# Performance work log

Hardware: AMD Instinct MI355X
Metric: run time of the kernel (lower is better)

The kernel has to match this reference:

```python
import jax, jax.numpy as jnp
import numpy as np

NEG_INF = -1e30  # stand-in for -inf in additive causal mask (softmax-safe)


def rotary_pos_emb(x):
    # x: [B, T, H, D]. Faithful to source: freqs = 1/1000**(arange(0,D,2)//D)
    # with INTEGER floor division -> exponent 0 -> all freqs == 1.0.
    B, T, H, D = x.shape
    exponents = (jnp.arange(0, D, 2)[: D // 2] // D).astype(jnp.float32)
    freqs = 1.0 / jnp.power(jnp.float32(1000.0), exponents)          # [D/2]
    theta = jnp.arange(T, dtype=jnp.float32)[:, None] * freqs[None, :]  # [T, D/2]
    cos = jnp.cos(theta)[None, :, None, :]  # [1, T, 1, D/2]
    sin = jnp.sin(theta)[None, :, None, :]
    xr = x.astype(jnp.float32).reshape(B, T, H, D // 2, 2)
    x0, x1 = xr[..., 0], xr[..., 1]
    # complex multiply (x0 + i x1) * (cos + i sin)
    out = jnp.stack([x0 * cos - x1 * sin, x0 * sin + x1 * cos], axis=-1)
    return out.reshape(B, T, H, D).astype(x.dtype)


def attention_fwd(x, wq, wk, wv, wo, n_heads=32):
    B, T, C = x.shape
    hd = C // n_heads  # head_dim = 128
    # nn.Linear(bias=False): y = x @ W^T with W: [out, in]
    xq = (x @ wq.T).reshape(B, T, n_heads, hd)
    xk = (x @ wk.T).reshape(B, T, n_heads, hd)
    xv = (x @ wv.T).reshape(B, T, n_heads, hd)
    xq = rotary_pos_emb(xq)
    xk = rotary_pos_emb(xk)
    # n_rep == 1 -> repeat_kv is identity
    scale = hd ** -0.5
    scores = jnp.einsum('bqhd,bkhd->bhqk', xq, xk) * scale  # [B,H,T,T]
    causal = jnp.tril(jnp.ones((T, T), dtype=bool))
    scores = jnp.where(causal[None, None], scores, NEG_INF)
    probs = jax.nn.softmax(scores.astype(jnp.float32), axis=-1).astype(xq.dtype)
    out = jnp.einsum('bhqk,bkhd->bqhd', probs, xv).reshape(B, T, C)
    return out @ wo.T


def setup_inputs() -> dict:
    key = jax.random.key(0)
    ks = jax.random.split(key, 5)
    B, T, C = 2, 2048, 4096
    s = 0.02
    return {
        'x': jax.random.normal(ks[0], (B, T, C), jnp.float32),
        'wq': jax.random.normal(ks[1], (C, C), jnp.float32) * s,
        'wk': jax.random.normal(ks[2], (C, C), jnp.float32) * s,
        'wv': jax.random.normal(ks[3], (C, C), jnp.float32) * s,
        'wo': jax.random.normal(ks[4], (C, C), jnp.float32) * s,
    }


def reference(x, wq, wk, wv, wo):
    return attention_fwd(x, wq, wk, wv, wo)
```

## Files before the change

kernel.cpp:

```cpp
#include <hip/hip_runtime.h>
#include <hip/hip_bf16.h>
#include <stdint.h>

typedef __bf16 bf16_t;
typedef __attribute__((ext_vector_type(8))) __bf16 bf16x8;
typedef __attribute__((ext_vector_type(4))) float f32x4;

#define GLL16(gptr, lptr)                                                      \
  __builtin_amdgcn_global_load_lds(                                            \
      (__attribute__((address_space(1))) void*)(gptr),                         \
      (__attribute__((address_space(3))) void*)(lptr), 16, 0, 0)

__global__ __launch_bounds__(256) void cast5_kernel(const float* __restrict__ x,
                                                    const float* __restrict__ wq,
                                                    const float* __restrict__ wk,
                                                    const float* __restrict__ wv,
                                                    const float* __restrict__ wo,
                                                    bf16_t* __restrict__ outbase) {
  const size_t SZ = (size_t)4096 * 4096;
  const float* in;
  switch (blockIdx.y) {
    case 0: in = x; break;
    case 1: in = wq; break;
    case 2: in = wk; break;
    case 3: in = wv; break;
    default: in = wo; break;
  }
  bf16_t* out = outbase + (size_t)blockIdx.y * SZ;
  int i = blockIdx.x * 256 + threadIdx.x;
  const float4* p = (const float4*)in + (size_t)i * 2;
  float4 a = p[0], b = p[1];
  bf16x8 o;
  o[0] = (__bf16)a.x; o[1] = (__bf16)a.y; o[2] = (__bf16)a.z; o[3] = (__bf16)a.w;
  o[4] = (__bf16)b.x; o[5] = (__bf16)b.y; o[6] = (__bf16)b.z; o[7] = (__bf16)b.w;
  *((bf16x8*)out + i) = o;
}

#define STAGE_HALF(gbase, ldsbase)                                             \
  do {                                                                         \
    GLL16((gbase) + (size_t)(w * 32 + sr) * 4096 + sq, (ldsbase) + w * 1024);  \
    GLL16((gbase) + (size_t)(w * 32 + 16 + sr) * 4096 + sq,                    \
          (ldsbase) + w * 1024 + 512);                                         \
  } while (0)

#define MFMA_CL(ACCB_, AF_, BF_)                                               \
  __builtin_amdgcn_sched_barrier(0);                                           \
  __builtin_amdgcn_s_setprio(1);                                               \
  _Pragma("unroll") for (int mi = 0; mi < 4; ++mi)                             \
      _Pragma("unroll") for (int ni = 0; ni < 4; ++ni)                         \
          acc[(ACCB_) + mi][ni] = __builtin_amdgcn_mfma_f32_16x16x32_bf16(     \
              AF_[mi], BF_[ni], acc[(ACCB_) + mi][ni], 0, 0, 0);               \
  __builtin_amdgcn_s_setprio(0);

#define KITER(P_, AF0C_, BFC_, AF0N_, BFN_, KT_, MORE_)                        \
  do {                                                                         \
    _Pragma("unroll") for (int mi = 0; mi < 4; ++mi) af1t[mi] =                \
        *(const bf16x8*)&As[P_][(wr * 128 + 64 + mi * 16 + l15) * 32 + sl8];   \
    MFMA_CL(0, AF0C_, BFC_)                                                    \
    asm volatile("s_waitcnt lgkmcnt(0)" ::: "memory");                         \
    __builtin_amdgcn_sched_barrier(0);                                         \
    __builtin_amdgcn_s_barrier();    \
    if (MORE_) {                                                               \
      STAGE_HALF(Ag + (size_t)(KT_ + 2) * 32, &As[P_][0]);                     \
      STAGE_HALF(Bg + (size_t)(KT_ + 2) * 32, &Bs[P_][0]);                     \
      asm volatile("s_waitcnt vmcnt(4)" ::: "memory");                         \
    } else {                                                                   \
      asm volatile("s_waitcnt vmcnt(0)" ::: "memory");                         \
    }                                                                          \
    __builtin_amdgcn_s_barrier();                \
    _Pragma("unroll") for (int ni = 0; ni < 4; ++ni) BFN_[ni] =                \
        *(const bf16x8*)&Bs[P_ ^ 1][(wc * 64 + ni * 16 + l15) * 32 + sl8];     \
    _Pragma("unroll") for (int mi = 0; mi < 4; ++mi) AF0N_[mi] =               \
        *(const bf16x8*)&As[P_ ^ 1][(wr * 128 + mi * 16 + l15) * 32 + sl8];    \
    MFMA_CL(4, af1t, BFC_)                                                     \
  } while (0)

#define GEMM256_MAIN(Aptr, Bptr)                                               \
  const bf16_t* Ag = (Aptr) + (size_t)bm * 4096;                               \
  const bf16_t* Bg = (Bptr) + (size_t)bn * 4096;                               \
  f32x4 acc[8][4] = {};                                                        \
  bf16x8 af0A[4], af0B[4], bfA[4], bfB[4], af1t[4];                            \
  STAGE_HALF(Ag, &As[0][0]);                                                   \
  STAGE_HALF(Bg, &Bs[0][0]);                                                   \
  STAGE_HALF(Ag + 32, &As[1][0]);                                              \
  STAGE_HALF(Bg + 32, &Bs[1][0]);                                              \
  asm volatile("s_waitcnt vmcnt(4)" ::: "memory");           \
  __builtin_amdgcn_s_barrier();                                                \
  _Pragma("unroll") for (int ni = 0; ni < 4; ++ni) bfA[ni] =                   \
      *(const bf16x8*)&Bs[0][(wc * 64 + ni * 16 + l15) * 32 + sl8];            \
  _Pragma("unroll") for (int mi = 0; mi < 4; ++mi) af0A[mi] =                  \
      *(const bf16x8*)&As[0][(wr * 128 + mi * 16 + l15) * 32 + sl8];           \
  for (int jj = 0; jj < 64; ++jj) {                                            \
    const int kt = jj * 2;                                                     \
    const bool m = (jj < 63);                                                  \
    KITER(0, af0A, bfA, af0B, bfB, kt, m);                                     \
    KITER(1, af0B, bfB, af0A, bfA, kt + 1, m);                                 \
  }

__device__ __forceinline__ void epi_rope256(const f32x4 (&acc)[8][4],
                                            bf16_t* __restrict__ C, int bm,
                                            int bn, int wr, int wc, int quad,
                                            int l15) {
#pragma unroll
  for (int a = 0; a < 8; ++a) {
    const int row0 = bm + wr * 128 + (a & 3) * 16 + (a >> 2) * 64 + quad * 4;
    float fsv[4], fcv[4];
#pragma unroll
    for (int r = 0; r < 4; ++r)
      sincosf((float)((row0 + r) & 2047), &fsv[r], &fcv[r]);
#pragma unroll
    for (int ni = 0; ni < 4; ++ni) {
      const int col = bn + wc * 64 + ni * 16 + l15;
      const bool odd = (col & 1);
#pragma unroll
      for (int r = 0; r < 4; ++r) {
        float v = acc[a][ni][r];
        float pr = __shfl_xor(v, 1, 64);
        float o = odd ? (pr * fsv[r] + v * fcv[r]) : (v * fcv[r] - pr * fsv[r]);
        C[(size_t)(row0 + r) * 4096 + col] = (__bf16)o;
      }
    }
  }
}

__device__ __forceinline__ void epi_vt256(const f32x4 (&acc)[8][4],
                                          bf16_t* __restrict__ VT, int bm,
                                          int bn, int wr, int wc, int quad,
                                          int l15) {
#pragma unroll
  for (int a = 0; a < 8; ++a) {
    const int row0 = bm + wr * 128 + (a & 3) * 16 + (a >> 2) * 64 + quad * 4;
    const int b = row0 >> 11, t0 = row0 & 2047;
#pragma unroll
    for (int ni = 0; ni < 4; ++ni) {
      const int col = bn + wc * 64 + ni * 16 + l15;
      const int h = col >> 7, d = col & 127;
      union { __bf16 e[4]; uint2 u; } pk;
#pragma unroll
      for (int r = 0; r < 4; ++r) pk.e[r] = (__bf16)acc[a][ni][r];
      *(uint2*)&VT[((size_t)((b * 32 + h) * 128 + d)) * 2048 + t0] = pk.u;
    }
  }
}

__global__ __launch_bounds__(512, 2) void gemm_qkv(const bf16_t* __restrict__ X,
                                                   const bf16_t* __restrict__ WQ,
                                                   const bf16_t* __restrict__ WK,
                                                   const bf16_t* __restrict__ WV,
                                                   bf16_t* __restrict__ Qo,
                                                   bf16_t* __restrict__ Ko,
                                                   bf16_t* __restrict__ VTo) {
  __shared__ bf16_t As[2][8192];
  __shared__ bf16_t Bs[2][8192];
  const int tid = threadIdx.x;
  const int w = tid >> 6;
  const int lane = tid & 63;
  const int quad = lane >> 4;
  const int l15 = lane & 15;
  const int wr = w >> 2, wc = w & 3;
  const int sr = lane >> 2;
  const int sq = (((lane & 3) ^ ((lane >> 3) & 3))) * 8;
  const int sl8 = (quad ^ ((l15 >> 1) & 3)) * 8;
  const int mat = blockIdx.y;
  int id = blockIdx.x;
  id = (id & 7) * 32 + (id >> 3);
  const int bm = (id >> 4) * 256, bn = (id & 15) * 256;
  const bf16_t* Bp = (mat == 0) ? WQ : (mat == 1) ? WK : WV;

  GEMM256_MAIN(X, Bp)

  if (mat == 0)
    epi_rope256(acc, Qo, bm, bn, wr, wc, quad, l15);
  else if (mat == 1)
    epi_rope256(acc, Ko, bm, bn, wr, wc, quad, l15);
  else
    epi_vt256(acc, VTo, bm, bn, wr, wc, quad, l15);
}

__global__ __launch_bounds__(512, 2) void gemm_out(const bf16_t* __restrict__ A,
                                                   const bf16_t* __restrict__ B,
                                                   float* __restrict__ C) {
  __shared__ bf16_t As[2][8192];
  __shared__ bf16_t Bs[2][8192];
  const int tid = threadIdx.x;
  const int w = tid >> 6;
  const int lane = tid & 63;
  const int quad = lane >> 4;
  const int l15 = lane & 15;
  const int wr = w >> 2, wc = w & 3;
  const int sr = lane >> 2;
  const int sq = (((lane & 3) ^ ((lane >> 3) & 3))) * 8;
  const int sl8 = (quad ^ ((l15 >> 1) & 3)) * 8;
  int id = blockIdx.x;
  id = (id & 7) * 32 + (id >> 3);
  const int bm = (id >> 4) * 256, bn = (id & 15) * 256;

  GEMM256_MAIN(A, B)

#pragma unroll
  for (int a = 0; a < 8; ++a) {
    const int row0 = bm + wr * 128 + (a & 3) * 16 + (a >> 2) * 64 + quad * 4;
#pragma unroll
    for (int ni = 0; ni < 4; ++ni) {
      const int col = bn + wc * 64 + ni * 16 + l15;
#pragma unroll
      for (int r = 0; r < 4; ++r)
        C[(size_t)(row0 + r) * 4096 + col] = acc[a][ni][r];
    }
  }
}

__global__ __launch_bounds__(256) void attn_kernel(const bf16_t* __restrict__ Q,
                                                   const bf16_t* __restrict__ Km,
                                                   const bf16_t* __restrict__ VT,
                                                   bf16_t* __restrict__ O) {
  __shared__ bf16_t Ks[64 * 128];
  __shared__ bf16_t Vts[128 * 64];
  __shared__ bf16_t QPs[64 * 128];
  const int tid = threadIdx.x;
  const int w = tid >> 6;
  const int lane = tid & 63;
  const int quad = lane >> 4;
  const int l15 = lane & 15;
  const int bh = blockIdx.x;
  const int qtile = 31 - blockIdx.y;
  const int mrow_base = (bh >> 5) * 2048;
  const int h = bh & 31;
  const float scale = 0.08838834764831845f;

#pragma unroll
  for (int it = 0; it < 4; ++it) {
    int c = w * 4 + it;
    int row = c * 4 + (lane >> 4);
    int cc = (lane & 15) ^ (row & 15);
    GLL16(Q + (size_t)(mrow_base + qtile * 64 + row) * 4096 + h * 128 + cc * 8,
          &QPs[c * 512]);
  }
  __syncthreads();
  bf16x8 qf[4];
#pragma unroll
  for (int ks = 0; ks < 4; ++ks) {
    int row = w * 16 + l15;
    int slot = (ks * 4 + quad) ^ (row & 15);
    qf[ks] = *(const bf16x8*)&QPs[row * 128 + slot * 8];
  }
  bf16_t* Pw = &QPs[w * 16 * 72];

  f32x4 accO[8] = {};
  float mrun[4], lrun[4];
#pragma unroll
  for (int r = 0; r < 4; ++r) { mrun[r] = -1e30f; lrun[r] = 0.f; }

  for (int kt = 0; kt <= qtile; ++kt) {
    __syncthreads();
#pragma unroll
    for (int it = 0; it < 4; ++it) {
      int c = w * 4 + it;
      int krow = c * 4 + (lane >> 4);
      int kcc = (lane & 15) ^ (krow & 15);
      GLL16(Km + (size_t)(mrow_base + kt * 64 + krow) * 4096 + h * 128 + kcc * 8,
            &Ks[c * 512]);
      int vrow = c * 8 + (lane >> 3);
      int vcc = (lane & 7) ^ (vrow & 7);
      GLL16(VT + (size_t)(bh * 128 + vrow) * 2048 + kt * 64 + vcc * 8,
            &Vts[c * 512]);
    }
    __syncthreads();

    f32x4 s[4];
#pragma unroll
    for (int ni = 0; ni < 4; ++ni) {
      s[ni] = (f32x4){0.f, 0.f, 0.f, 0.f};
#pragma unroll
      for (int ks = 0; ks < 4; ++ks) {
        int row = ni * 16 + l15;
        int slot = (ks * 4 + quad) ^ (row & 15);
        bf16x8 kf = *(const bf16x8*)&Ks[row * 128 + slot * 8];
        s[ni] = __builtin_amdgcn_mfma_f32_16x16x32_bf16(qf[ks], kf, s[ni], 0, 0, 0);
      }
    }
    const bool diag = (kt == qtile);
#pragma unroll
    for (int ni = 0; ni < 4; ++ni)
#pragma unroll
      for (int r = 0; r < 4; ++r) {
        float v = s[ni][r] * scale;
        if (diag && (ni * 16 + l15) > (w * 16 + quad * 4 + r)) v = -1e30f;
        s[ni][r] = v;
      }
    float mx[4], alpha[4], rs[4];
#pragma unroll
    for (int r = 0; r < 4; ++r)
      mx[r] = fmaxf(fmaxf(s[0][r], s[1][r]), fmaxf(s[2][r], s[3][r]));
#pragma unroll
    for (int off = 1; off < 16; off <<= 1)
#pragma unroll
      for (int r = 0; r < 4; ++r) mx[r] = fmaxf(mx[r], __shfl_xor(mx[r], off, 64));
    float ps[4][4];
#pragma unroll
    for (int r = 0; r < 4; ++r) {
      float mn = fmaxf(mrun[r], mx[r]);
      alpha[r] = __expf(mrun[r] - mn);
      mrun[r] = mn;
      rs[r] = 0.f;
    }
#pragma unroll
    for (int ni = 0; ni < 4; ++ni)
#pragma unroll
      for (int r = 0; r < 4; ++r) {
        float p = __expf(s[ni][r] - mrun[r]);
        ps[ni][r] = p;
        rs[r] += p;
      }
#pragma unroll
    for (int off = 1; off < 16; off <<= 1)
#pragma unroll
      for (int r = 0; r < 4; ++r) rs[r] += __shfl_xor(rs[r], off, 64);
#pragma unroll
    for (int r = 0; r < 4; ++r) lrun[r] = lrun[r] * alpha[r] + rs[r];
#pragma unroll
    for (int nt = 0; nt < 8; ++nt)
#pragma unroll
      for (int r = 0; r < 4; ++r) accO[nt][r] *= alpha[r];
#pragma unroll
    for (int ni = 0; ni < 4; ++ni)
#pragma unroll
      for (int r = 0; r < 4; ++r)
        Pw[(quad * 4 + r) * 72 + ni * 16 + l15] = (__bf16)ps[ni][r];
    asm volatile("s_waitcnt lgkmcnt(0)" ::: "memory");
    bf16x8 pf[2];
#pragma unroll
    for (int ks = 0; ks < 2; ++ks)
      pf[ks] = *(const bf16x8*)&Pw[l15 * 72 + ks * 32 + quad * 8];
#pragma unroll
    for (int nt = 0; nt < 8; ++nt)
#pragma unroll
      for (int ks = 0; ks < 2; ++ks) {
        int vrow = nt * 16 + l15;
        int slot = (ks * 4 + quad) ^ (vrow & 7);
        bf16x8 vf = *(const bf16x8*)&Vts[vrow * 64 + slot * 8];
        accO[nt] = __builtin_amdgcn_mfma_f32_16x16x32_bf16(pf[ks], vf, accO[nt], 0, 0, 0);
      }
  }

#pragma unroll
  for (int r = 0; r < 4; ++r) lrun[r] = 1.f / lrun[r];
#pragma unroll
  for (int nt = 0; nt < 8; ++nt)
#pragma unroll
    for (int r = 0; r < 4; ++r) {
      int trow = qtile * 64 + w * 16 + quad * 4 + r;
      int d = nt * 16 + l15;
      O[(size_t)(mrow_base + trow) * 4096 + h * 128 + d] =
          (__bf16)(accO[nt][r] * lrun[r]);
    }
}

extern "C" void kernel_launch(void* const* d_in, const int* in_sizes, int n_in,
                              void* d_out, int out_size, void* d_ws, size_t ws_size,
                              hipStream_t stream) {
  (void)in_sizes; (void)n_in; (void)out_size; (void)ws_size;
  const float* x = (const float*)d_in[0];
  const float* wq = (const float*)d_in[1];
  const float* wk = (const float*)d_in[2];
  const float* wv = (const float*)d_in[3];
  const float* wo = (const float*)d_in[4];
  float* out = (float*)d_out;

  const size_t SZ = (size_t)4096 * 4096;
  bf16_t* xb = (bf16_t*)d_ws;
  bf16_t* wqb = xb + SZ;
  bf16_t* wkb = wqb + SZ;
  bf16_t* wvb = wkb + SZ;
  bf16_t* wob = wvb + SZ;
  bf16_t* qb = wob + SZ;
  bf16_t* kb = qb + SZ;
  bf16_t* vtb = kb + SZ;
  bf16_t* ab = vtb + SZ;

  dim3 b256(256), b512(512);
  cast5_kernel<<<dim3((unsigned)(SZ / 8 / 256), 5), b256, 0, stream>>>(
      x, wq, wk, wv, wo, xb);

  gemm_qkv<<<dim3(256, 3), b512, 0, stream>>>(xb, wqb, wkb, wvb, qb, kb, vtb);

  attn_kernel<<<dim3(64, 32), b256, 0, stream>>>(qb, kb, vtb, ab);

  gemm_out<<<dim3(256), b512, 0, stream>>>(ab, wob, out);
}
```

Measured before the change: 1.117 ms.

## Deepen GEMM LDS pipeline to four stages with one barrier per k-step

The shared GEMM main loop moves from a two-slot LDS double buffer to a four-slot ring that prefetches three k-tiles ahead. Each k-step now issues a single workgroup barrier instead of two, and a partial lgkmcnt wait lets the first MFMA cluster start before all fragment loads finish. The goal is to hide more global-load latency and cut barrier stalls in both the QKV and output projection GEMMs. The cost is doubled LDS per block (128 KB), which likely allows only one 512-thread block per CU instead of the two the launch bounds target.

```diff
diff --git a/kernel.cpp b/kernel.cpp
--- a/kernel.cpp
+++ b/kernel.cpp
@@ -43,36 +43,39 @@
           (ldsbase) + w * 1024 + 512);                                         \
   } while (0)
 
-#define MFMA_CL(ACCB_, AF_, BF_)                                               \
-  __builtin_amdgcn_sched_barrier(0);                                           \
-  __builtin_amdgcn_s_setprio(1);                                               \
+#define MFMA16(ACCB_, AF_, BF_)                                                \
   _Pragma("unroll") for (int mi = 0; mi < 4; ++mi)                             \
       _Pragma("unroll") for (int ni = 0; ni < 4; ++ni)                         \
           acc[(ACCB_) + mi][ni] = __builtin_amdgcn_mfma_f32_16x16x32_bf16(     \
-              AF_[mi], BF_[ni], acc[(ACCB_) + mi][ni], 0, 0, 0);               \
-  __builtin_amdgcn_s_setprio(0);
-
-#define KITER(P_, AF0C_, BFC_, AF0N_, BFN_, KT_, MORE_)                        \
+              AF_[mi], BF_[ni], acc[(ACCB_) + mi][ni], 0, 0, 0)
+
+#define KSTEP(SLOT_, AFC_, BFC_, AFN_, BFN_, STAGE_STMT, VMCNT_STMT, LAST_)    \
   do {                                                                         \
     _Pragma("unroll") for (int mi = 0; mi < 4; ++mi) af1t[mi] =                \
-        *(const bf16x8*)&As[P_][(wr * 128 + 64 + mi * 16 + l15) * 32 + sl8];   \
-    MFMA_CL(0, AF0C_, BFC_)                                                    \
+        *(const bf16x8*)&As[SLOT_][(wr * 128 + 64 + mi * 16 + l15) * 32 + sl8];\
+    asm volatile("s_waitcnt lgkmcnt(4)" ::: "memory");                         \
+    __builtin_amdgcn_sched_barrier(0);                                         \
+    __builtin_amdgcn_s_setprio(1);                                             \
+    MFMA16(0, AFC_, BFC_);                                                     \
+    __builtin_amdgcn_s_setprio(0);                                             \
+    __builtin_amdgcn_sched_barrier(0);                                         \
+    STAGE_STMT;                                                                \
     asm volatile("s_waitcnt lgkmcnt(0)" ::: "memory");                         \
+    VMCNT_STMT;                                                                \
     __builtin_amdgcn_sched_barrier(0);                                         \
-    __builtin_amdgcn_s_barrier();    \
-    if (MORE_) {                                                               \
-      STAGE_HALF(Ag + (size_t)(KT_ + 2) * 32, &As[P_][0]);                     \
-      STAGE_HALF(Bg + (size_t)(KT_ + 2) * 32, &Bs[P_][0]);                     \
-      asm volatile("s_waitcnt vmcnt(4)" ::: "memory");                         \
-    } else {                                                                   \
-      asm volatile("s_waitcnt vmcnt(0)" ::: "memory");                         \
+    if (!(LAST_)) {                                                            \
+      __builtin_amdgcn_s_barrier();                                            \
+      _Pragma("unroll") for (int ni = 0; ni < 4; ++ni) BFN_[ni] =              \
+          *(const bf16x8*)&Bs[(SLOT_ + 1) & 3][(wc * 64 + ni * 16 + l15) * 32 +\
+                                               sl8];                           \
+      _Pragma("unroll") for (int mi = 0; mi < 4; ++mi) AFN_[mi] =              \
+          *(const bf16x8*)&As[(SLOT_ + 1) & 3][(wr * 128 + mi * 16 + l15) * 32 \
+                                               + sl8];                         \
     }                                                                          \
-    __builtin_amdgcn_s_barrier();                \
-    _Pragma("unroll") for (int ni = 0; ni < 4; ++ni) BFN_[ni] =                \
-        *(const bf16x8*)&Bs[P_ ^ 1][(wc * 64 + ni * 16 + l15) * 32 + sl8];     \
-    _Pragma("unroll") for (int mi = 0; mi < 4; ++mi) AF0N_[mi] =               \
-        *(const bf16x8*)&As[P_ ^ 1][(wr * 128 + mi * 16 + l15) * 32 + sl8];    \
-    MFMA_CL(4, af1t, BFC_)                                                     \
+    __builtin_amdgcn_sched_barrier(0);                                         \
+    __builtin_amdgcn_s_setprio(1);                                             \
+    MFMA16(4, af1t, BFC_);                                                     \
+    __builtin_amdgcn_s_setprio(0);                                             \
   } while (0)
 
 #define GEMM256_MAIN(Aptr, Bptr)                                               \
@@ -84,18 +87,42 @@
   STAGE_HALF(Bg, &Bs[0][0]);                                                   \
   STAGE_HALF(Ag + 32, &As[1][0]);                                              \
   STAGE_HALF(Bg + 32, &Bs[1][0]);                                              \
-  asm volatile("s_waitcnt vmcnt(4)" ::: "memory");           \
+  STAGE_HALF(Ag + 64, &As[2][0]);                                              \
+  STAGE_HALF(Bg + 64, &Bs[2][0]);                                              \
+  asm volatile("s_waitcnt vmcnt(8)" ::: "memory");           \
   __builtin_amdgcn_s_barrier();                                                \
   _Pragma("unroll") for (int ni = 0; ni < 4; ++ni) bfA[ni] =                   \
       *(const bf16x8*)&Bs[0][(wc * 64 + ni * 16 + l15) * 32 + sl8];            \
   _Pragma("unroll") for (int mi = 0; mi < 4; ++mi) af0A[mi] =                  \
       *(const bf16x8*)&As[0][(wr * 128 + mi * 16 + l15) * 32 + sl8];           \
-  for (int jj = 0; jj < 64; ++jj) {                                            \
-    const int kt = jj * 2;                                                     \
-    const bool m = (jj < 63);                                                  \
-    KITER(0, af0A, bfA, af0B, bfB, kt, m);                                     \
-    KITER(1, af0B, bfB, af0A, bfA, kt + 1, m);                                 \
-  }
+  for (int jj = 0; jj < 31; ++jj) {                                            \
+    const int kt = jj * 4;                                                     \
+    KSTEP(0, af0A, bfA, af0B, bfB,                                             \
+          { STAGE_HALF(Ag + (size_t)(kt + 3) * 32, &As[3][0]);                 \
+            STAGE_HALF(Bg + (size_t)(kt + 3) * 32, &Bs[3][0]); },              \
+          asm volatile("s_waitcnt vmcnt(8)" ::: "memory"), 0);                 \
+    KSTEP(1, af0B, bfB, af0A, bfA,                                             \
+          { STAGE_HALF(Ag + (size_t)(kt + 4) * 32, &As[0][0]);                 \
+            STAGE_HALF(Bg + (size_t)(kt + 4) * 32, &Bs[0][0]); },              \
+          asm volatile("s_waitcnt vmcnt(8)" ::: "memory"), 0);                 \
+    KSTEP(2, af0A, bfA, af0B, bfB,                                             \
+          { STAGE_HALF(Ag + (size_t)(kt + 5) * 32, &As[1][0]);                 \
+            STAGE_HALF(Bg + (size_t)(kt + 5) * 32, &Bs[1][0]); },              \
+          asm volatile("s_waitcnt vmcnt(8)" ::: "memory"), 0);                 \
+    KSTEP(3, af0B, bfB, af0A, bfA,                                             \
+          { STAGE_HALF(Ag + (size_t)(kt + 6) * 32, &As[2][0]);                 \
+            STAGE_HALF(Bg + (size_t)(kt + 6) * 32, &Bs[2][0]); },              \
+          asm volatile("s_waitcnt vmcnt(8)" ::: "memory"), 0);                 \
+  }                                                                            \
+  KSTEP(0, af0A, bfA, af0B, bfB,                                               \
+        { STAGE_HALF(Ag + (size_t)127 * 32, &As[3][0]);                        \
+          STAGE_HALF(Bg + (size_t)127 * 32, &Bs[3][0]); },                     \
+        asm volatile("s_waitcnt vmcnt(8)" ::: "memory"), 0);        \
+  KSTEP(1, af0B, bfB, af0A, bfA, (void)0,                                      \
+        asm volatile("s_waitcnt vmcnt(4)" ::: "memory"), 0);        \
+  KSTEP(2, af0A, bfA, af0B, bfB, (void)0,                                      \
+        asm volatile("s_waitcnt vmcnt(0)" ::: "memory"), 0);        \
+  KSTEP(3, af0B, bfB, af0A, bfA, (void)0, (void)0, 1);
 
 __device__ __forceinline__ void epi_rope256(const f32x4 (&acc)[8][4],
                                             bf16_t* __restrict__ C, int bm,
@@ -150,8 +177,8 @@
                                                    bf16_t* __restrict__ Qo,
                                                    bf16_t* __restrict__ Ko,
                                                    bf16_t* __restrict__ VTo) {
-  __shared__ bf16_t As[2][8192];
-  __shared__ bf16_t Bs[2][8192];
+  __shared__ bf16_t As[4][8192];
+  __shared__ bf16_t Bs[4][8192];
   const int tid = threadIdx.x;
   const int w = tid >> 6;
   const int lane = tid & 63;
@@ -180,8 +207,8 @@
 __global__ __launch_bounds__(512, 2) void gemm_out(const bf16_t* __restrict__ A,
                                                    const bf16_t* __restrict__ B,
                                                    float* __restrict__ C) {
-  __shared__ bf16_t As[2][8192];
-  __shared__ bf16_t Bs[2][8192];
+  __shared__ bf16_t As[4][8192];
+  __shared__ bf16_t Bs[4][8192];
   const int tid = threadIdx.x;
   const int w = tid >> 6;
   const int lane = tid & 63;
```

New measurement: 978.7 us. -12.4%, faster.
